# Kernel optimization log

Hardware: AMD Instinct MI355X
Metric: run time of the kernel (lower is better)

The kernel has to match this reference:

```python
import jax, jax.numpy as jnp
import numpy as np

NUM_GRAPHS = 512   # number of graphs in the batch
MAX_NODES = 192    # static pad bound (actual sizes are in [96,160])
TOTAL = 65536      # total atoms across all graphs
D = 256            # model dim (from MultiheadAttention(256, 4))
H = 4              # heads
DH = D // H        # head dim = 64


def setup_inputs() -> dict:
    # Ragged graph sizes that sum exactly to TOTAL (pairs 128+p / 128-p).
    rng = np.random.default_rng(0)
    p = rng.integers(0, 33, size=NUM_GRAPHS // 2)
    sizes = np.concatenate([128 + p, 128 - p])
    rng.shuffle(sizes)
    batch = np.repeat(np.arange(NUM_GRAPHS, dtype=np.int32), sizes)

    key = jax.random.key(0)
    ks = jax.random.split(key, 12)
    s = 0.02
    return {
        "x": jax.random.normal(ks[0], (TOTAL, D), jnp.float32),
        "batch": jnp.asarray(batch),
        # attn1 (torch MultiheadAttention packed in_proj + out_proj)
        "in_w1": jax.random.normal(ks[1], (3 * D, D), jnp.float32) * s,
        "in_b1": jnp.zeros((3 * D,), jnp.float32),
        "out_w1": jax.random.normal(ks[2], (D, D), jnp.float32) * s,
        "out_b1": jnp.zeros((D,), jnp.float32),
        # attn2
        "in_w2": jax.random.normal(ks[3], (3 * D, D), jnp.float32) * s,
        "in_b2": jnp.zeros((3 * D,), jnp.float32),
        "out_w2": jax.random.normal(ks[4], (D, D), jnp.float32) * s,
        "out_b2": jnp.zeros((D,), jnp.float32),
        # readout MLP: 256 -> 256 -> 128 -> 1 (dropout is identity in eval)
        "r_w1": jax.random.normal(ks[5], (256, 256), jnp.float32) * s,
        "r_b1": jnp.zeros((256,), jnp.float32),
        "r_w2": jax.random.normal(ks[6], (128, 256), jnp.float32) * s,
        "r_b2": jnp.zeros((128,), jnp.float32),
        "r_w3": jax.random.normal(ks[7], (1, 128), jnp.float32) * s,
        "r_b3": jnp.zeros((1,), jnp.float32),
    }


def _mha(xd, mask, in_w, in_b, out_w, out_b):
    # xd: [B, L, D], mask: [B, L] (True = valid key). torch MHA semantics.
    B, L, _ = xd.shape
    qkv = xd @ in_w.T + in_b                                  # [B, L, 3D]
    q, k, v = jnp.split(qkv, 3, axis=-1)
    split = lambda t: t.reshape(B, L, H, DH).transpose(0, 2, 1, 3)  # [B,H,L,DH]
    q, k, v = split(q), split(k), split(v)
    scores = jnp.einsum("bhqd,bhkd->bhqk", q, k) / jnp.sqrt(jnp.float32(DH))
    scores = jnp.where(mask[:, None, None, :], scores, -jnp.inf)
    attn = jax.nn.softmax(scores, axis=-1)                    # each graph has >=1 node
    o = jnp.einsum("bhqk,bhkd->bhqd", attn, v)                # [B,H,L,DH]
    o = o.transpose(0, 2, 1, 3).reshape(B, L, D)
    return o @ out_w.T + out_b


def reference(x, batch, in_w1, in_b1, out_w1, out_b1,
              in_w2, in_b2, out_w2, out_b2,
              r_w1, r_b1, r_w2, r_b2, r_w3, r_b3):
    # Scatter ragged atoms into a padded dense [B, MAX_NODES, D] block
    # (equivalent to the per-graph Python loop, but one fused pass).
    idx = jnp.arange(TOTAL)
    pos = idx - jnp.searchsorted(batch, batch, side="left")   # position within graph
    dense = jnp.zeros((NUM_GRAPHS, MAX_NODES, D), x.dtype).at[batch, pos].set(x)
    mask = jnp.zeros((NUM_GRAPHS, MAX_NODES), bool).at[batch, pos].set(True)

    h = _mha(dense, mask, in_w1, in_b1, out_w1, out_b1)
    h = _mha(h, mask, in_w2, in_b2, out_w2, out_b2)

    # masked mean-pool over valid nodes of each graph
    m = mask[..., None].astype(h.dtype)
    pooled = (h * m).sum(axis=1) / m.sum(axis=1)              # [B, D]

    h1 = jax.nn.relu(pooled @ r_w1.T + r_b1)                  # dropout = identity (eval)
    h2 = jax.nn.relu(h1 @ r_w2.T + r_b2)
    energy = h2 @ r_w3.T + r_b3                               # [B, 1]
    return energy[:, 0]                                       # (batch_size,)
```

## Files before the change

### kernel.cpp

```cpp
#include <hip/hip_runtime.h>
#include <math.h>

#define TOTAL 65536
#define NG 512
#define DMODEL 256
#define QKVLD 768

typedef __attribute__((ext_vector_type(8))) short bf16x8;
typedef __attribute__((ext_vector_type(4))) float f32x4;

__device__ inline ushort f2bf(float f) {
    unsigned int u = __float_as_uint(f);
    unsigned int r = (u + 0x7FFFu + ((u >> 16) & 1u)) >> 16;
    return (ushort)r;
}
__device__ inline float bf2f(ushort h) { return __uint_as_float(((unsigned int)h) << 16); }

__device__ __forceinline__ void llds16(const void* gptr, void* lptr) {
    __builtin_amdgcn_global_load_lds(
        (const __attribute__((address_space(1))) unsigned int*)gptr,
        (__attribute__((address_space(3))) unsigned int*)lptr, 16, 0, 0);
}

__global__ __launch_bounds__(256) void prep_kernel(
    const float* __restrict__ x, const float* __restrict__ in_w1,
    const float* __restrict__ in_w2, const float* __restrict__ out_w1,
    const float* __restrict__ out_b1, const float* __restrict__ in_b2,
    const int* __restrict__ batch,
    ushort* __restrict__ xb, ushort* __restrict__ Wb1,
    ushort* __restrict__ Wc2b, float* __restrict__ bc2, int* __restrict__ starts)
{
    const int b = blockIdx.x, t = threadIdx.x;
    if (b < 16384) {
        int i = b * 256 + t;
        float4 v = ((const float4*)x)[i];
        ushort4 u;
        u.x = f2bf(v.x); u.y = f2bf(v.y); u.z = f2bf(v.z); u.w = f2bf(v.w);
        ((ushort4*)xb)[i] = u;
    } else if (b < 16576) {
        int i = (b - 16384) * 256 + t;
        float4 v = ((const float4*)in_w1)[i];
        ushort4 u;
        u.x = f2bf(v.x); u.y = f2bf(v.y); u.z = f2bf(v.z); u.w = f2bf(v.w);
        ((ushort4*)Wb1)[i] = u;
    } else if (b < 17344) {
        const int n = b - 16576;
        __shared__ float wrow[256];
        wrow[t] = in_w2[n * 256 + t];
        __syncthreads();
        float s = 0.f;
#pragma unroll 8
        for (int j = 0; j < 256; ++j) s += wrow[j] * out_w1[j * 256 + t];
        Wc2b[n * 256 + t] = f2bf(s);
    } else if (b < 17347) {
        int n = (b - 17344) * 256 + t;
        if (n < 768) {
            float s = 0.f;
            for (int j = 0; j < 256; ++j) s += in_w2[n * 256 + j] * out_b1[j];
            bc2[n] = s + in_b2[n];
        }
    } else {
        int g = (b - 17347) * 256 + t;
        if (g < NG) {
            int lo = 0, hi = TOTAL;
            while (lo < hi) {
                int mid = (lo + hi) >> 1;
                if (batch[mid] < g) lo = mid + 1; else hi = mid;
            }
            starts[g] = lo;
            if (g == 0) starts[NG] = TOTAL;
        }
    }
}

__global__ __launch_bounds__(256) void gemm_mfma(
    const ushort* __restrict__ A,
    const ushort* __restrict__ W,
    const float* __restrict__ bias,
    ushort* __restrict__ C, int ldc)
{
    __shared__ ushort As[128 * 64];
    __shared__ ushort Bs[128 * 64];
    const int tid = threadIdx.x;
    const int lane = tid & 63, wid = tid >> 6;
    const int grp = lane >> 4, ln16 = lane & 15;
    const int wm = wid & 1, wn = wid >> 1;

    const int bid = blockIdx.x;
    const int xcd = bid & 7;
    const int j6  = bid >> 3;
    const int mt  = xcd * 64 + j6 / 6;
    const int nt  = j6 % 6;
    const int n0 = nt * 128, m0 = mt * 128;

    const int lrow = lane >> 3;
    const int lchunk = (lane & 7) ^ lrow;

    f32x4 acc[4][4];
#pragma unroll
    for (int i = 0; i < 4; ++i)
#pragma unroll
        for (int j = 0; j < 4; ++j) acc[i][j] = (f32x4){0.f, 0.f, 0.f, 0.f};

    for (int k0 = 0; k0 < 256; k0 += 64) {
#pragma unroll
        for (int j = 0; j < 4; ++j) {
            int band = wid * 32 + j * 8;
            int row = band + lrow;
            llds16(A + (size_t)(m0 + row) * 256 + k0 + lchunk * 8, &As[band * 64]);
            llds16(W + (size_t)(n0 + row) * 256 + k0 + lchunk * 8, &Bs[band * 64]);
        }
        __syncthreads();
#pragma unroll
        for (int kc = 0; kc < 2; ++kc) {
            bf16x8 a[4], b[4];
#pragma unroll
            for (int i = 0; i < 4; ++i) {
                int r = wm * 64 + i * 16 + ln16;
                int p = (kc * 4 + grp) ^ (r & 7);
                a[i] = *(const bf16x8*)&As[r * 64 + p * 8];
            }
#pragma unroll
            for (int j = 0; j < 4; ++j) {
                int r = wn * 64 + j * 16 + ln16;
                int p = (kc * 4 + grp) ^ (r & 7);
                b[j] = *(const bf16x8*)&Bs[r * 64 + p * 8];
            }
#pragma unroll
            for (int i = 0; i < 4; ++i)
#pragma unroll
                for (int j = 0; j < 4; ++j)
                    acc[i][j] = __builtin_amdgcn_mfma_f32_16x16x32_bf16(a[i], b[j], acc[i][j], 0, 0, 0);
        }
        __syncthreads();
    }

#pragma unroll
    for (int j = 0; j < 4; ++j) {
        int col = n0 + wn * 64 + j * 16 + ln16;
        float bv = bias[col];
#pragma unroll
        for (int i = 0; i < 4; ++i) {
            int r0 = m0 + wm * 64 + i * 16 + grp * 4;
#pragma unroll
            for (int reg = 0; reg < 4; ++reg)
                C[(size_t)(r0 + reg) * ldc + col] = f2bf(acc[i][j][reg] + bv);
        }
    }
}

#define VLD 168
#define PLD 72

__global__ __launch_bounds__(256) void attn_mfma(const ushort* __restrict__ qkv,
                                                 ushort* __restrict__ obuf,
                                                 float* __restrict__ psumOut,
                                                 const int* __restrict__ starts) {
    __shared__ ushort Ks[160 * 64];
    __shared__ ushort Vt[64 * VLD];
    __shared__ ushort Ps[4 * 16 * PLD];
    __shared__ float  red[4][64];
    const int g = blockIdx.x;
    const int h = blockIdx.y;
    int s = starts[g];
    int e = starts[g + 1];
    s = (s < 0) ? 0 : ((s > TOTAL) ? TOTAL : s);
    e = (e < s) ? s : ((e > TOTAL) ? TOTAL : e);
    int L = e - s;
    if (L > 160) L = 160;
    if (L < 1) L = 1;
    const int tid = threadIdx.x;
    const int lane = tid & 63, wid = tid >> 6;
    const int grp = lane >> 4, ln16 = lane & 15;
    const int lrow = lane >> 3;
    const int lchunk = (lane & 7) ^ lrow;

#pragma unroll
    for (int r = 0; r < 5; ++r) {
        int band = (r * 4 + wid) * 8;
        int row = band + lrow;
        int crow = (row < L) ? row : (L - 1);
        llds16(qkv + (size_t)(s + crow) * QKVLD + 256 + h * 64 + lchunk * 8, &Ks[band * 64]);
    }
#pragma unroll
    for (int r = 0; r < 5; ++r) {
        int idx = r * 256 + tid;
        int kc = idx >> 6;
        int d = idx & 63;
        ushort tmp[8];
#pragma unroll
        for (int j = 0; j < 8; ++j) {
            int key = kc * 8 + j;
            int ckey = (key < L) ? key : (L - 1);
            tmp[j] = qkv[(size_t)(s + ckey) * QKVLD + 512 + h * 64 + d];
        }
        *(uint4*)&Vt[d * VLD + kc * 8] = *(const uint4*)tmp;
    }
    __syncthreads();

    ushort* myP = &Ps[wid * 16 * PLD];
    float psum[4] = {0.f, 0.f, 0.f, 0.f};
    const bool pooled = (psumOut != nullptr);

    for (int q0 = wid * 16; q0 < L; q0 += 64) {
        bf16x8 qa[2];
        {
            int qi = q0 + ln16;
            int grow = (qi < L) ? (s + qi) : s;
            const ushort* qbase = qkv + (size_t)grow * QKVLD + h * 64;
            qa[0] = *(const bf16x8*)(qbase + grp * 8);
            qa[1] = *(const bf16x8*)(qbase + 32 + grp * 8);
        }
        f32x4 sc[10];
#pragma unroll
        for (int kt = 0; kt < 10; ++kt) {
            int row = kt * 16 + ln16;
            int p0 = grp ^ (row & 7);
            int p1 = (4 + grp) ^ (row & 7);
            bf16x8 b0 = *(const bf16x8*)&Ks[row * 64 + p0 * 8];
            bf16x8 b1 = *(const bf16x8*)&Ks[row * 64 + p1 * 8];
            f32x4 z = (f32x4){0.f, 0.f, 0.f, 0.f};
            z = __builtin_amdgcn_mfma_f32_16x16x32_bf16(qa[0], b0, z, 0, 0, 0);
            z = __builtin_amdgcn_mfma_f32_16x16x32_bf16(qa[1], b1, z, 0, 0, 0);
            sc[kt] = z;
        }
        float sm[4] = {0.f, 0.f, 0.f, 0.f};
#pragma unroll
        for (int kt = 0; kt < 10; ++kt) {
            bool dead = (kt * 16 + ln16) >= L;
#pragma unroll
            for (int r = 0; r < 4; ++r) {
                float p = __expf(dead ? -INFINITY : sc[kt][r] * 0.125f);
                sc[kt][r] = p;
                sm[r] += p;
            }
        }
#pragma unroll
        for (int m = 1; m <= 8; m <<= 1)
#pragma unroll
            for (int r = 0; r < 4; ++r) sm[r] += __shfl_xor(sm[r], m, 64);
        float inv[4];
#pragma unroll
        for (int r = 0; r < 4; ++r) inv[r] = 1.f / sm[r];

        f32x4 o[4];
#pragma unroll
        for (int dt = 0; dt < 4; ++dt) o[dt] = (f32x4){0.f, 0.f, 0.f, 0.f};
#pragma unroll
        for (int st = 0; st < 3; ++st) {
            const int nkt = (st == 2) ? 2 : 4;
            const int nkc = (st == 2) ? 1 : 2;
#pragma unroll
            for (int kti = 0; kti < 4; ++kti) {
                if (kti < nkt) {
                    int kt = st * 4 + kti;
#pragma unroll
                    for (int r = 0; r < 4; ++r)
                        myP[(grp * 4 + r) * PLD + kti * 16 + ln16] = f2bf(sc[kt][r]);
                }
            }
#pragma unroll
            for (int kc2 = 0; kc2 < 2; ++kc2) {
                if (kc2 < nkc) {
                    bf16x8 pa = *(const bf16x8*)&myP[ln16 * PLD + kc2 * 32 + grp * 8];
                    int kcg = st * 2 + kc2;
#pragma unroll
                    for (int dt = 0; dt < 4; ++dt) {
                        bf16x8 vb = *(const bf16x8*)&Vt[(dt * 16 + ln16) * VLD + kcg * 32 + grp * 8];
                        o[dt] = __builtin_amdgcn_mfma_f32_16x16x32_bf16(pa, vb, o[dt], 0, 0, 0);
                    }
                }
            }
        }
        if (pooled) {
#pragma unroll
            for (int dt = 0; dt < 4; ++dt)
#pragma unroll
                for (int reg = 0; reg < 4; ++reg) {
                    int q = q0 + grp * 4 + reg;
                    if (q < L) psum[dt] += o[dt][reg] * inv[reg];
                }
        } else {
#pragma unroll
            for (int dt = 0; dt < 4; ++dt)
#pragma unroll
                for (int reg = 0; reg < 4; ++reg) {
                    int q = q0 + grp * 4 + reg;
                    if (q < L)
                        obuf[(size_t)(s + q) * DMODEL + h * 64 + dt * 16 + ln16] =
                            f2bf(o[dt][reg] * inv[reg]);
                }
        }
    }

    if (pooled) {
#pragma unroll
        for (int dt = 0; dt < 4; ++dt) {
            psum[dt] += __shfl_xor(psum[dt], 16, 64);
            psum[dt] += __shfl_xor(psum[dt], 32, 64);
        }
        if (grp == 0) {
#pragma unroll
            for (int dt = 0; dt < 4; ++dt) red[wid][dt * 16 + ln16] = psum[dt];
        }
        __syncthreads();
        if (tid < 64) {
            float v = red[0][tid] + red[1][tid] + red[2][tid] + red[3][tid];
            psumOut[g * DMODEL + h * 64 + tid] = v;
        }
    }
}

__global__ __launch_bounds__(256) void readout_kernel(
    const float* __restrict__ psum, const int* __restrict__ starts,
    const float* __restrict__ ow2, const float* __restrict__ ob2,
    const float* __restrict__ w1, const float* __restrict__ b1,
    const float* __restrict__ w2, const float* __restrict__ b2,
    const float* __restrict__ w3, const float* __restrict__ b3,
    float* __restrict__ out)
{
    __shared__ float xs[256], ps[256], h1s[256], h2s[128];
    const int g = blockIdx.x, t = threadIdx.x;
    int s = starts[g], e = starts[g + 1];
    s = (s < 0) ? 0 : ((s > TOTAL) ? TOTAL : s);
    e = (e < s) ? s : ((e > TOTAL) ? TOTAL : e);
    int L = e - s;
    if (L < 1) L = 1;
    xs[t] = psum[g * 256 + t] / (float)L;
    __syncthreads();
    {
        const float* wr = ow2 + t * 256;
        float s0 = 0.f;
#pragma unroll 8
        for (int i = 0; i < 256; ++i) s0 += xs[i] * wr[i];
        ps[t] = s0 + ob2[t];
    }
    __syncthreads();
    {
        const float* wr = w1 + t * 256;
        float s0 = 0.f;
#pragma unroll 8
        for (int i = 0; i < 256; ++i) s0 += ps[i] * wr[i];
        float v = s0 + b1[t];
        h1s[t] = v > 0.f ? v : 0.f;
    }
    __syncthreads();
    if (t < 128) {
        const float* wr = w2 + t * 256;
        float s0 = 0.f;
#pragma unroll 8
        for (int i = 0; i < 256; ++i) s0 += h1s[i] * wr[i];
        float v = s0 + b2[t];
        h2s[t] = v > 0.f ? v : 0.f;
    }
    __syncthreads();
    if (t < 64) {
        float v = h2s[t] * w3[t] + h2s[t + 64] * w3[t + 64];
#pragma unroll
        for (int off = 32; off > 0; off >>= 1) v += __shfl_down(v, off, 64);
        if (t == 0) out[g] = v + b3[0];
    }
}

__global__ __launch_bounds__(256) void zero_out_kernel(float* __restrict__ out, int n) {
    int i = blockIdx.x * 256 + threadIdx.x;
    if (i < n) out[i] = 0.f;
}

extern "C" void kernel_launch(void* const* d_in, const int* in_sizes, int n_in,
                              void* d_out, int out_size, void* d_ws, size_t ws_size,
                              hipStream_t stream) {
    float* out = (float*)d_out;

    const int expect[16] = {
        TOTAL * DMODEL, TOTAL,
        3 * DMODEL * DMODEL, 3 * DMODEL,
        DMODEL * DMODEL, DMODEL,
        3 * DMODEL * DMODEL, 3 * DMODEL,
        DMODEL * DMODEL, DMODEL,
        256 * 256, 256,
        128 * 256, 128,
        128, 1
    };
    const size_t NEEDED = 135536640ull;
    bool ok = (n_in == 16) && (out_size == NG) && (d_ws != nullptr) && (ws_size >= NEEDED);
    if (ok) {
        for (int i = 0; i < 16; ++i)
            if (in_sizes[i] != expect[i]) { ok = false; break; }
    }
    if (!ok) {
        zero_out_kernel<<<(out_size + 255) / 256, 256, 0, stream>>>(out, out_size);
        return;
    }

    const float* x      = (const float*)d_in[0];
    const int*   batch  = (const int*)d_in[1];
    const float* in_w1  = (const float*)d_in[2];
    const float* in_b1  = (const float*)d_in[3];
    const float* out_w1 = (const float*)d_in[4];
    const float* out_b1 = (const float*)d_in[5];
    const float* in_w2  = (const float*)d_in[6];
    const float* in_b2  = (const float*)d_in[7];
    const float* out_w2 = (const float*)d_in[8];
    const float* out_b2 = (const float*)d_in[9];
    const float* r_w1   = (const float*)d_in[10];
    const float* r_b1   = (const float*)d_in[11];
    const float* r_w2   = (const float*)d_in[12];
    const float* r_b2   = (const float*)d_in[13];
    const float* r_w3   = (const float*)d_in[14];
    const float* r_b3   = (const float*)d_in[15];

    char* ws = (char*)d_ws;
    int*    starts = (int*)(ws + 0);
    float*  bc2    = (float*)(ws + 4096);
    float*  psum   = (float*)(ws + 8192);
    ushort* Wc2b   = (ushort*)(ws + 532480);
    ushort* Wb1    = (ushort*)(ws + 925696);
    ushort* bufO   = (ushort*)(ws + 1318912);
    ushort* bufQKV = (ushort*)(ws + 34873344ull);

    prep_kernel<<<17349, 256, 0, stream>>>(x, in_w1, in_w2, out_w1, out_b1, in_b2,
                                           batch, bufO, Wb1, Wc2b, bc2, starts);

    gemm_mfma<<<3072, 256, 0, stream>>>(bufO, Wb1, in_b1, bufQKV, QKVLD);
    attn_mfma<<<dim3(NG, 4), 256, 0, stream>>>(bufQKV, bufO, nullptr, starts);

    gemm_mfma<<<3072, 256, 0, stream>>>(bufO, Wc2b, bc2, bufQKV, QKVLD);
    attn_mfma<<<dim3(NG, 4), 256, 0, stream>>>(bufQKV, bufO, psum, starts);

    readout_kernel<<<NG, 256, 0, stream>>>(psum, starts, out_w2, out_b2,
                                           r_w1, r_b1, r_w2, r_b2, r_w3, r_b3, out);
}
```

Baseline: 340.7 us.

## Read K directly from global, swizzle V tile, defer barrier, add setprio

The attention kernel no longer stages K into shared memory. Each wave now loads its K fragments straight from global memory (clamped to valid rows) inside the QK loop, which frees the Ks buffer and lets the first score computation overlap the V transpose. The block barrier moves to after the first softmax. The V tile gets an XOR swizzle, with its row stride widened to fit the swizzled range, to reduce LDS bank conflicts. s_setprio raises wave priority around the MFMA sections. In exchange, every wave re-reads K from global/L2 for each query tile, which exposes more memory latency in the QK loop.

```diff
diff --git a/kernel.cpp b/kernel.cpp
--- a/kernel.cpp
+++ b/kernel.cpp
@@ -149,14 +149,13 @@
     }
 }
 
-#define VLD 168
+#define VLD 192
 #define PLD 72
 
 __global__ __launch_bounds__(256) void attn_mfma(const ushort* __restrict__ qkv,
                                                  ushort* __restrict__ obuf,
                                                  float* __restrict__ psumOut,
                                                  const int* __restrict__ starts) {
-    __shared__ ushort Ks[160 * 64];
     __shared__ ushort Vt[64 * VLD];
     __shared__ ushort Ps[4 * 16 * PLD];
     __shared__ float  red[4][64];
@@ -172,16 +171,7 @@
     const int tid = threadIdx.x;
     const int lane = tid & 63, wid = tid >> 6;
     const int grp = lane >> 4, ln16 = lane & 15;
-    const int lrow = lane >> 3;
-    const int lchunk = (lane & 7) ^ lrow;
-
-#pragma unroll
-    for (int r = 0; r < 5; ++r) {
-        int band = (r * 4 + wid) * 8;
-        int row = band + lrow;
-        int crow = (row < L) ? row : (L - 1);
-        llds16(qkv + (size_t)(s + crow) * QKVLD + 256 + h * 64 + lchunk * 8, &Ks[band * 64]);
-    }
+
 #pragma unroll
     for (int r = 0; r < 5; ++r) {
         int idx = r * 256 + tid;
@@ -194,14 +184,15 @@
             int ckey = (key < L) ? key : (L - 1);
             tmp[j] = qkv[(size_t)(s + ckey) * QKVLD + 512 + h * 64 + d];
         }
-        *(uint4*)&Vt[d * VLD + kc * 8] = *(const uint4*)tmp;
-    }
-    __syncthreads();
+        *(uint4*)&Vt[d * VLD + ((kc ^ (d & 7)) * 8)] = *(const uint4*)tmp;
+    }
 
     ushort* myP = &Ps[wid * 16 * PLD];
     float psum[4] = {0.f, 0.f, 0.f, 0.f};
     const bool pooled = (psumOut != nullptr);
-
+    const ushort* kbase = qkv + (size_t)s * QKVLD + 256 + h * 64 + grp * 8;
+
+    bool first = true;
     for (int q0 = wid * 16; q0 < L; q0 += 64) {
         bf16x8 qa[2];
         {
@@ -212,18 +203,20 @@
             qa[1] = *(const bf16x8*)(qbase + 32 + grp * 8);
         }
         f32x4 sc[10];
+        __builtin_amdgcn_s_setprio(1);
 #pragma unroll
         for (int kt = 0; kt < 10; ++kt) {
-            int row = kt * 16 + ln16;
-            int p0 = grp ^ (row & 7);
-            int p1 = (4 + grp) ^ (row & 7);
-            bf16x8 b0 = *(const bf16x8*)&Ks[row * 64 + p0 * 8];
-            bf16x8 b1 = *(const bf16x8*)&Ks[row * 64 + p1 * 8];
+            int key = kt * 16 + ln16;
+            int ck = (key < L) ? key : (L - 1);
+            const ushort* kp = kbase + (size_t)ck * QKVLD;
+            bf16x8 b0 = *(const bf16x8*)kp;
+            bf16x8 b1 = *(const bf16x8*)(kp + 32);
             f32x4 z = (f32x4){0.f, 0.f, 0.f, 0.f};
             z = __builtin_amdgcn_mfma_f32_16x16x32_bf16(qa[0], b0, z, 0, 0, 0);
             z = __builtin_amdgcn_mfma_f32_16x16x32_bf16(qa[1], b1, z, 0, 0, 0);
             sc[kt] = z;
         }
+        __builtin_amdgcn_s_setprio(0);
         float sm[4] = {0.f, 0.f, 0.f, 0.f};
 #pragma unroll
         for (int kt = 0; kt < 10; ++kt) {
@@ -243,6 +236,8 @@
 #pragma unroll
         for (int r = 0; r < 4; ++r) inv[r] = 1.f / sm[r];
 
+        if (first) { __syncthreads(); first = false; }
+
         f32x4 o[4];
 #pragma unroll
         for (int dt = 0; dt < 4; ++dt) o[dt] = (f32x4){0.f, 0.f, 0.f, 0.f};
@@ -259,6 +254,7 @@
                         myP[(grp * 4 + r) * PLD + kti * 16 + ln16] = f2bf(sc[kt][r]);
                 }
             }
+            __builtin_amdgcn_s_setprio(1);
 #pragma unroll
             for (int kc2 = 0; kc2 < 2; ++kc2) {
                 if (kc2 < nkc) {
@@ -266,11 +262,13 @@
                     int kcg = st * 2 + kc2;
 #pragma unroll
                     for (int dt = 0; dt < 4; ++dt) {
-                        bf16x8 vb = *(const bf16x8*)&Vt[(dt * 16 + ln16) * VLD + kcg * 32 + grp * 8];
+                        bf16x8 vb = *(const bf16x8*)
+                            &Vt[(dt * 16 + ln16) * VLD + (((kcg * 4 + grp) ^ (ln16 & 7)) * 8)];
                         o[dt] = __builtin_amdgcn_mfma_f32_16x16x32_bf16(pa, vb, o[dt], 0, 0, 0);
                     }
                 }
             }
+            __builtin_amdgcn_s_setprio(0);
         }
         if (pooled) {
 #pragma unroll
```

Result: slower. 389.1 us (+14.2%).
